# Performance work log

Measured on AMD Instinct MI355X. Metric: run time of the kernel, lower is better.

## Reference

```python
import jax, jax.numpy as jnp
import numpy as np

N = 20000      # nodes per batched graph
E = 320000     # directed edges per batched graph
F_IN = 128     # num_features
H = 256        # nhid == each gnn filter
G = 128        # number of graphs in batch


def setup_inputs() -> dict:
    key = jax.random.key(0)
    ks = jax.random.split(key, 24)

    def glorot(k, shape):
        fan_in, fan_out = shape[0], shape[1]
        limit = np.sqrt(6.0 / (fan_in + fan_out)).astype(np.float32)
        return jax.random.uniform(k, shape, jnp.float32, -limit, limit)

    inp = {
        'x1': jax.random.normal(ks[0], (N, F_IN), jnp.float32),
        'x2': jax.random.normal(ks[1], (N, F_IN), jnp.float32),
        'edge_index1': jax.random.randint(ks[2], (2, E), 0, N),
        'edge_index2': jax.random.randint(ks[3], (2, E), 0, N),
        'batch1': jnp.sort(jax.random.randint(ks[4], (N,), 0, G)),
        'batch2': jnp.sort(jax.random.randint(ks[5], (N,), 0, G)),
        # GCN layer weights (shared between the two graphs, as in the module)
        'W0': glorot(ks[6], (F_IN, H)), 'b0': jnp.zeros((H,), jnp.float32),
        'W1': glorot(ks[7], (H, H)),    'b1': jnp.zeros((H,), jnp.float32),
        'W2': glorot(ks[8], (H, H)),    'b2': jnp.zeros((H,), jnp.float32),
        # MLP head: nhid*2 -> nhid -> nhid//2 -> 1
        'lw0': glorot(ks[9], (2 * H, H)),      'lb0': jnp.zeros((H,), jnp.float32),
        'lw1': glorot(ks[10], (H, H // 2)),    'lb1': jnp.zeros((H // 2,), jnp.float32),
        'lw2': glorot(ks[11], (H // 2, 1)),    'lb2': jnp.zeros((1,), jnp.float32),
    }
    return inp


def _gcn_conv(x, src, dst, W, b, n):
    """PyG GCNConv: x' = D^-1/2 (A + I) D^-1/2 (x W) + b (self-loops added)."""
    x = x @ W                                      # [N, out]
    loop = jnp.arange(n)
    s = jnp.concatenate([src, loop])               # sources incl. self-loops
    d = jnp.concatenate([dst, loop])               # targets incl. self-loops
    deg = jax.ops.segment_sum(jnp.ones(s.shape, jnp.float32), d, num_segments=n)
    dinv = jnp.where(deg > 0, deg ** -0.5, 0.0)
    norm = dinv[s] * dinv[d]                       # [E+N]
    out = jax.ops.segment_sum(x[s] * norm[:, None], d, num_segments=n)
    return out + b


def _encode(x, edge_index, batch, params):
    src, dst = edge_index[0], edge_index[1]
    n = x.shape[0]
    for (W, b) in params:
        # conv -> relu -> dropout(eval: identity)
        x = jax.nn.relu(_gcn_conv(x, src, dst, W, b, n))
    # global_add_pool
    return jax.ops.segment_sum(x, batch, num_segments=G)   # [G, H]


def reference(x1, x2, W0, b0, W1, b1, W2, b2,
              lw0, lb0, lw1, lb1, lw2, lb2,
              edge_index1, edge_index2, batch1, batch2):
    params = ((W0, b0), (W1, b1), (W2, b2))
    g1 = _encode(x1, edge_index1, batch1, params)
    g2 = _encode(x2, edge_index2, batch2, params)
    scores = jnp.concatenate([g1, g2], axis=1)              # [G, 2H]
    h = jax.nn.relu(scores @ lw0 + lb0)
    h = jax.nn.relu(h @ lw1 + lb1)
    return jax.nn.sigmoid(h @ lw2 + lb2).reshape(-1)        # [G]
```

## Files before the change

kernel.cpp:

```cpp
#include <hip/hip_runtime.h>
#include <hip/hip_bf16.h>
#include <math.h>

#define HD 256
#define GB 128

typedef __attribute__((ext_vector_type(8))) short bf16x8;
typedef __attribute__((ext_vector_type(4))) float f32x4;
typedef __attribute__((ext_vector_type(2))) float f32x2;

__device__ __forceinline__ float bf2f(unsigned short u) {
  return __uint_as_float(((unsigned int)u) << 16);
}
__device__ __forceinline__ unsigned short f2bf(float f) {
  unsigned int u = __float_as_uint(f);
  unsigned int r = u + 0x7FFFu + ((u >> 16) & 1u);
  return (unsigned short)(r >> 16);
}

__device__ __forceinline__ float f8dec(unsigned u) {
  unsigned s = (u >> 7) & 1u, e = (u >> 3) & 15u, m = u & 7u;
  float mag = e ? __uint_as_float(((e + 120u) << 23) | (m << 20))
                : (float)m * 0.001953125f;
  return s ? -mag : mag;
}
__device__ __forceinline__ unsigned f8enc(float x) {
#if __has_builtin(__builtin_amdgcn_cvt_pk_fp8_f32)
  return (unsigned)__builtin_amdgcn_cvt_pk_fp8_f32(x, x, 0, false) & 0xFFu;
#else
  float a = fabsf(x);
  unsigned s = x < 0.f ? 0x80u : 0u;
  if (a >= 440.f) return s | 0x7Eu;
  if (a < 0.015625f) {
    int q = (int)rintf(a * 512.f);
    return s | (unsigned)q;
  }
  unsigned u = __float_as_uint(a);
  u += 0x7FFFFu + ((u >> 20) & 1u);
  unsigned e = (u >> 23) - 120u;
  if (e >= 16u) return s | 0x7Eu;
  return s | (e << 3) | ((u >> 20) & 7u);
#endif
}

template<int FB>
__device__ __forceinline__ void load_row_f8(const unsigned char* p, float (&f)[FB]) {
  if constexpr (FB == 4) {
    unsigned u = *(const unsigned*)p;
#if __has_builtin(__builtin_amdgcn_cvt_pk_f32_fp8)
    f32x2 lo = __builtin_amdgcn_cvt_pk_f32_fp8((int)u, false);
    f32x2 hi = __builtin_amdgcn_cvt_pk_f32_fp8((int)u, true);
    f[0] = lo[0]; f[1] = lo[1]; f[2] = hi[0]; f[3] = hi[1];
#else
    f[0] = f8dec(u); f[1] = f8dec(u >> 8); f[2] = f8dec(u >> 16); f[3] = f8dec(u >> 24);
#endif
  } else {
    unsigned u = *(const unsigned short*)p;
#if __has_builtin(__builtin_amdgcn_cvt_pk_f32_fp8)
    f32x2 lo = __builtin_amdgcn_cvt_pk_f32_fp8((int)u, false);
    f[0] = lo[0]; f[1] = lo[1];
#else
    f[0] = f8dec(u); f[1] = f8dec(u >> 8);
#endif
  }
}

__global__ __launch_bounds__(256) void k_prep(const float* __restrict__ W0, const float* __restrict__ W1,
                                              const float* __restrict__ W2,
                                              unsigned short* __restrict__ Wt0,
                                              unsigned short* __restrict__ Wt1,
                                              unsigned short* __restrict__ Wt2,
                                              const float4* __restrict__ x1, const float4* __restrict__ x2,
                                              unsigned* __restrict__ x8, int n4,
                                              float* __restrict__ scores, int* __restrict__ deg, int nd) {
  int i = blockIdx.x * blockDim.x + threadIdx.x;
  if (i < 163840) {
    const float* W; unsigned short* Wt; int j;
    if (i < 32768)      { W = W0; Wt = Wt0; j = i; }
    else if (i < 98304) { W = W1; Wt = Wt1; j = i - 32768; }
    else                { W = W2; Wt = Wt2; j = i - 98304; }
    int k = j >> 8, c = j & 255;
    Wt[(((size_t)(k >> 3) * HD) + c) * 8 + (k & 7)] = f2bf(W[(size_t)k * HD + c]);
    return;
  }
  int j = i - 163840;
  if (j < 2 * n4) {
    float4 v = (j < n4) ? x1[j] : x2[j - n4];
    x8[j] = f8enc(v.x) | (f8enc(v.y) << 8) | (f8enc(v.z) << 16) | (f8enc(v.w) << 24);
    return;
  }
  j -= 2 * n4;
  if (j < GB * 512) { scores[j] = 0.f; return; }
  j -= GB * 512;
  if (j < nd) deg[j] = 0;
}

__global__ void k_deg2(const int* __restrict__ dst1, const int* __restrict__ dst2,
                       int* __restrict__ deg, int e, int n0) {
  int i = blockIdx.x * blockDim.x + threadIdx.x;
  if (i >= 2 * e) return;
  int d = (i < e) ? dst1[i] : (dst2[i - e] + n0);
  atomicAdd(&deg[d], 1);
}

__global__ __launch_bounds__(256) void k_scan_a(const int* __restrict__ deg,
                                                int* __restrict__ partial, int n) {
  __shared__ int sh[256];
  int i = blockIdx.x * 256 + threadIdx.x;
  int v = (i < n) ? deg[i] : 0;
  sh[threadIdx.x] = v;
  __syncthreads();
#pragma unroll
  for (int off = 128; off; off >>= 1) {
    if (threadIdx.x < off) sh[threadIdx.x] += sh[threadIdx.x + off];
    __syncthreads();
  }
  if (threadIdx.x == 0) partial[blockIdx.x] = sh[0];
}

__global__ __launch_bounds__(256) void k_scan_b(int* __restrict__ partial, int nb,
                                                int* __restrict__ row_ptr, int n, int e_total) {
  __shared__ int sh[256];
  int t = threadIdx.x;
  int v = (t < nb) ? partial[t] : 0;
  sh[t] = v;
  __syncthreads();
#pragma unroll
  for (int off = 1; off < 256; off <<= 1) {
    int u = (t >= off) ? sh[t - off] : 0;
    __syncthreads();
    sh[t] += u;
    __syncthreads();
  }
  if (t < nb) partial[t] = sh[t] - v;
  if (t == 0) row_ptr[n] = e_total;
}

__global__ __launch_bounds__(256) void k_scan_c(const int* __restrict__ deg,
                                                const int* __restrict__ partial,
                                                int* __restrict__ row_ptr,
                                                float* __restrict__ dinv,
                                                int* __restrict__ cursor, int n) {
  __shared__ int sh[256];
  int i = blockIdx.x * 256 + threadIdx.x;
  int t = threadIdx.x;
  int v = (i < n) ? deg[i] : 0;
  sh[t] = v;
  __syncthreads();
#pragma unroll
  for (int off = 1; off < 256; off <<= 1) {
    int u = (t >= off) ? sh[t - off] : 0;
    __syncthreads();
    sh[t] += u;
    __syncthreads();
  }
  if (i < n) {
    row_ptr[i] = sh[t] - v + partial[blockIdx.x];
    dinv[i] = rsqrtf((float)(v + 1));
    cursor[i] = 0;
  }
}

__global__ void k_build2(const int* __restrict__ ei1, const int* __restrict__ ei2,
                         const float* __restrict__ dinv, const int* __restrict__ row_ptr,
                         int* __restrict__ cursor, int2* __restrict__ csr, int e, int n0) {
  int i = blockIdx.x * blockDim.x + threadIdx.x;
  if (i >= 2 * e) return;
  int s, d;
  if (i < e) { s = ei1[i];          d = ei1[i + e]; }
  else       { s = ei2[i - e] + n0; d = ei2[i] + n0; }
  int pos = atomicAdd(&cursor[d], 1);
  int idx = row_ptr[d] + pos;
  csr[idx] = make_int2(s, __float_as_int(dinv[s] * dinv[d]));
}

template<bool BR, bool F8OUT>
__global__ __launch_bounds__(256) void k_gemm_bf(const unsigned short* __restrict__ A,
                                                 const unsigned short* __restrict__ Wt,
                                                 const float* __restrict__ bias,
                                                 void* __restrict__ Cv,
                                                 int K) {
  const int w = threadIdx.x >> 6;
  const int lane = threadIdx.x & 63;
  const int bm = blockIdx.x * 64 + w * 16;
  const int bn = blockIdx.y * 128;
  const int row = bm + (lane & 15);
  const int kg0 = lane >> 4;
  f32x4 acc[8];
#pragma unroll
  for (int i = 0; i < 8; ++i) acc[i] = (f32x4){0.f, 0.f, 0.f, 0.f};

  const unsigned short* arow = A + (size_t)row * K + kg0 * 8;
  for (int k0 = 0; k0 < K; k0 += 32) {
    bf16x8 a = *(const bf16x8*)(arow + k0);
    const unsigned short* bbase =
        Wt + (((size_t)((k0 >> 3) + kg0) * HD) + bn + (lane & 15)) * 8;
#pragma unroll
    for (int nt = 0; nt < 8; ++nt) {
      bf16x8 b = *(const bf16x8*)(bbase + (size_t)nt * 16 * 8);
      acc[nt] = __builtin_amdgcn_mfma_f32_16x16x32_bf16(a, b, acc[nt], 0, 0, 0);
    }
  }
  const int crow = bm + (lane >> 4) * 4;
  const int ccol = bn + (lane & 15);
#pragma unroll
  for (int nt = 0; nt < 8; ++nt) {
    float bb = BR ? bias[ccol + nt * 16] : 0.f;
#pragma unroll
    for (int r = 0; r < 4; ++r) {
      float v = acc[nt][r];
      if (BR) v = fmaxf(v + bb, 0.f);
      size_t idx = (size_t)(crow + r) * HD + ccol + nt * 16;
      if constexpr (F8OUT) ((unsigned char*)Cv)[idx] = (unsigned char)f8enc(v);
      else                 ((unsigned short*)Cv)[idx] = f2bf(v);
    }
  }
}

template<int FB, bool BR>
__global__ __launch_bounds__(256) void k_gathf8(const unsigned char* __restrict__ y,
                                                const int* __restrict__ row_ptr,
                                                const int2* __restrict__ csr,
                                                const float* __restrict__ dinv,
                                                const float* __restrict__ bias,
                                                unsigned short* __restrict__ out, int n) {
  constexpr int F = FB * 64;
  int node = (blockIdx.x * blockDim.x + threadIdx.x) >> 6;
  int lane = threadIdx.x & 63;
  if (node >= n) return;
  float di = dinv[node];
  float c = di * di;
  float self[FB], acc0[FB], acc1[FB];
  load_row_f8<FB>(y + (size_t)node * F + lane * FB, self);
#pragma unroll
  for (int q = 0; q < FB; ++q) { acc0[q] = c * self[q]; acc1[q] = 0.f; }

  int e = row_ptr[node], end = row_ptr[node + 1];
  while (e < end) {
    int cnt = min(end - e, 64);
    int2 ew = make_int2(0, 0);
    if (lane < cnt) ew = csr[e + lane];
    int j = 0;
    for (; j + 4 <= cnt; j += 4) {
      int s0 = __shfl(ew.x, j + 0), s1 = __shfl(ew.x, j + 1);
      int s2 = __shfl(ew.x, j + 2), s3 = __shfl(ew.x, j + 3);
      float w0 = __int_as_float(__shfl(ew.y, j + 0));
      float w1 = __int_as_float(__shfl(ew.y, j + 1));
      float w2 = __int_as_float(__shfl(ew.y, j + 2));
      float w3 = __int_as_float(__shfl(ew.y, j + 3));
      float r0[FB], r1[FB], r2[FB], r3[FB];
      load_row_f8<FB>(y + (size_t)s0 * F + lane * FB, r0);
      load_row_f8<FB>(y + (size_t)s1 * F + lane * FB, r1);
      load_row_f8<FB>(y + (size_t)s2 * F + lane * FB, r2);
      load_row_f8<FB>(y + (size_t)s3 * F + lane * FB, r3);
#pragma unroll
      for (int q = 0; q < FB; ++q) {
        acc0[q] = fmaf(w0, r0[q], acc0[q]);
        acc1[q] = fmaf(w1, r1[q], acc1[q]);
        acc0[q] = fmaf(w2, r2[q], acc0[q]);
        acc1[q] = fmaf(w3, r3[q], acc1[q]);
      }
    }
    for (; j < cnt; ++j) {
      int s0 = __shfl(ew.x, j);
      float w0 = __int_as_float(__shfl(ew.y, j));
      float r0[FB];
      load_row_f8<FB>(y + (size_t)s0 * F + lane * FB, r0);
#pragma unroll
      for (int q = 0; q < FB; ++q) acc0[q] = fmaf(w0, r0[q], acc0[q]);
    }
    e += cnt;
  }
  unsigned short o[FB];
#pragma unroll
  for (int q = 0; q < FB; ++q) {
    float v = acc0[q] + acc1[q];
    if (BR) v = fmaxf(v + bias[lane * FB + q], 0.f);
    o[q] = f2bf(v);
  }
  if constexpr (FB == 4) {
    ushort4 ov; ov.x = o[0]; ov.y = o[1]; ov.z = o[2]; ov.w = o[3];
    *(ushort4*)(out + (size_t)node * F + lane * FB) = ov;
  } else {
    ushort2 ov; ov.x = o[0]; ov.y = o[1];
    *(ushort2*)(out + (size_t)node * F + lane * FB) = ov;
  }
}

__global__ __launch_bounds__(256) void k_pool4(const unsigned short* __restrict__ h,
                                               const int* __restrict__ batch1,
                                               const int* __restrict__ batch2,
                                               float* __restrict__ scores,
                                               int n, int n0) {
  int wave = (blockIdx.x * blockDim.x + threadIdx.x) >> 6;
  int lane = threadIdx.x & 63;
  int beg = wave * 32;
  if (beg >= n) return;
  int end = min(beg + 32, n);
  bool g1 = beg >= n0;
  const int* bat = g1 ? batch2 : batch1;
  int boff = g1 ? n0 : 0;
  int coff = g1 ? HD : 0;
  float ax = 0.f, ay = 0.f, az = 0.f, aw = 0.f;
  int cur = bat[beg - boff];
  for (int i = beg; i < end; ++i) {
    int b = bat[i - boff];
    if (b != cur) {
      float* srow = &scores[(size_t)cur * 512 + coff + lane * 4];
      atomicAdd(&srow[0], ax); atomicAdd(&srow[1], ay);
      atomicAdd(&srow[2], az); atomicAdd(&srow[3], aw);
      ax = ay = az = aw = 0.f;
      cur = b;
    }
    ushort4 v = reinterpret_cast<const ushort4*>(h + (size_t)i * HD)[lane];
    ax += bf2f(v.x); ay += bf2f(v.y); az += bf2f(v.z); aw += bf2f(v.w);
  }
  float* srow = &scores[(size_t)cur * 512 + coff + lane * 4];
  atomicAdd(&srow[0], ax); atomicAdd(&srow[1], ay);
  atomicAdd(&srow[2], az); atomicAdd(&srow[3], aw);
}

__global__ __launch_bounds__(256) void k_head_a(const float* __restrict__ scores,
                                                const float* __restrict__ lw0,
                                                const float* __restrict__ lb0,
                                                float* __restrict__ h1) {
  __shared__ float s_in[512];
  __shared__ float part[4][64];
  const int r = blockIdx.x, ct = blockIdx.y;
  const int t = threadIdx.x;
  s_in[t]       = scores[(size_t)r * 512 + t];
  s_in[t + 256] = scores[(size_t)r * 512 + t + 256];
  __syncthreads();
  const int l = t & 63, w = t >> 6;
  const int col = ct * 64 + l;
  float acc = 0.f;
  const float* wp = lw0 + (size_t)(w * 128) * 256 + col;
  const float* sp = s_in + w * 128;
#pragma unroll 8
  for (int k = 0; k < 128; ++k) acc = fmaf(sp[k], wp[(size_t)k * 256], acc);
  part[w][l] = acc;
  __syncthreads();
  if (t < 64) {
    float v = part[0][t] + part[1][t] + part[2][t] + part[3][t] + lb0[ct * 64 + t];
    h1[(size_t)r * 256 + ct * 64 + t] = fmaxf(v, 0.f);
  }
}

__global__ __launch_bounds__(256) void k_head_b(const float* __restrict__ h1,
                                                const float* __restrict__ lw1,
                                                const float* __restrict__ lb1,
                                                const float* __restrict__ lw2,
                                                const float* __restrict__ lb2,
                                                float* __restrict__ out) {
  __shared__ float s_in[256];
  __shared__ float part[2][128];
  __shared__ float s_h2[128];
  __shared__ float red[4];
  const int r = blockIdx.x;
  const int t = threadIdx.x;
  s_in[t] = h1[(size_t)r * 256 + t];
  __syncthreads();
  const int l = t & 127, w = t >> 7;
  float acc = 0.f;
  const float* wp = lw1 + (size_t)(w * 128) * 128 + l;
  const float* sp = s_in + w * 128;
#pragma unroll 8
  for (int k = 0; k < 128; ++k) acc = fmaf(sp[k], wp[(size_t)k * 128], acc);
  part[w][l] = acc;
  __syncthreads();
  if (t < 128) s_h2[t] = fmaxf(part[0][t] + part[1][t] + lb1[t], 0.f);
  __syncthreads();
  float p = (t < 128) ? s_h2[t] * lw2[t] : 0.f;
#pragma unroll
  for (int off = 32; off; off >>= 1) p += __shfl_down(p, off);
  if ((t & 63) == 0) red[t >> 6] = p;
  __syncthreads();
  if (t == 0) {
    float z = red[0] + red[1] + red[2] + red[3] + lb2[0];
    out[r] = 1.f / (1.f + expf(-z));
  }
}

extern "C" void kernel_launch(void* const* d_in, const int* in_sizes, int n_in,
                              void* d_out, int out_size, void* d_ws, size_t ws_size,
                              hipStream_t stream) {
  const float* x1 = (const float*)d_in[0];
  const float* x2 = (const float*)d_in[1];
  const int* ei1 = (const int*)d_in[2];
  const int* ei2 = (const int*)d_in[3];
  const int* batch1 = (const int*)d_in[4];
  const int* batch2 = (const int*)d_in[5];
  const float* W0 = (const float*)d_in[6];  const float* b0 = (const float*)d_in[7];
  const float* W1 = (const float*)d_in[8];  const float* b1 = (const float*)d_in[9];
  const float* W2 = (const float*)d_in[10]; const float* b2 = (const float*)d_in[11];
  const float* lw0 = (const float*)d_in[12]; const float* lb0 = (const float*)d_in[13];
  const float* lw1 = (const float*)d_in[14]; const float* lb1 = (const float*)d_in[15];
  const float* lw2 = (const float*)d_in[16]; const float* lb2 = (const float*)d_in[17];
  float* out = (float*)d_out;

  const int N = in_sizes[0] / 128;
  const int E = in_sizes[2] / 2;
  const int N2 = 2 * N, E2 = 2 * E;
  const int NB = (N2 + 255) / 256;

  char* p = (char*)d_ws;
  unsigned char*  x8   = (unsigned char*)p;  p += (size_t)N2 * 128;
  unsigned short* aggx = (unsigned short*)p; p += (size_t)N2 * 128 * 2;
  unsigned short* h    = (unsigned short*)p; p += (size_t)N2 * HD * 2;
  unsigned char*  y    = (unsigned char*)p;  p += (size_t)N2 * HD;
  unsigned short* Wt0  = (unsigned short*)p; p += (size_t)128 * HD * 2;
  unsigned short* Wt1  = (unsigned short*)p; p += (size_t)HD * HD * 2;
  unsigned short* Wt2  = (unsigned short*)p; p += (size_t)HD * HD * 2;
  float* dinv   = (float*)p; p += (size_t)N2 * 4;
  float* scores = (float*)p; p += (size_t)GB * 512 * 4;
  float* h1     = (float*)p; p += (size_t)GB * 256 * 4;
  int2* csr    = (int2*)p; p += (size_t)E2 * 8;
  int* deg     = (int*)p; p += (size_t)N2 * 4;
  int* row_ptr = (int*)p; p += (size_t)(N2 + 1) * 4;
  int* cursor  = (int*)p; p += (size_t)N2 * 4;
  int* partial = (int*)p; p += 256 * 4;

  int n4 = N * 128 / 4;
  int prep_total = 163840 + 2 * n4 + GB * 512 + N2;
  k_prep<<<(prep_total + 255) / 256, 256, 0, stream>>>(
      W0, W1, W2, Wt0, Wt1, Wt2,
      (const float4*)x1, (const float4*)x2, (unsigned*)x8, n4, scores, deg, N2);

  k_deg2<<<(2 * E + 255) / 256, 256, 0, stream>>>(ei1 + E, ei2 + E, deg, E, N);
  k_scan_a<<<NB, 256, 0, stream>>>(deg, partial, N2);
  k_scan_b<<<1, 256, 0, stream>>>(partial, NB, row_ptr, N2, E2);
  k_scan_c<<<NB, 256, 0, stream>>>(deg, partial, row_ptr, dinv, cursor, N2);
  k_build2<<<(2 * E + 255) / 256, 256, 0, stream>>>(ei1, ei2, dinv, row_ptr,
                                                    cursor, csr, E, N);

  dim3 ggrid(N2 / 64, 2);
  k_gathf8<2, false><<<(N2 + 3) / 4, 256, 0, stream>>>(x8, row_ptr, csr, dinv,
                                                       nullptr, aggx, N2);
  k_gemm_bf<true, false><<<ggrid, 256, 0, stream>>>(aggx, Wt0, b0, h, 128);
  k_gemm_bf<false, true><<<ggrid, 256, 0, stream>>>(h, Wt1, nullptr, y, HD);
  k_gathf8<4, true><<<(N2 + 3) / 4, 256, 0, stream>>>(y, row_ptr, csr, dinv,
                                                      b1, h, N2);
  k_gemm_bf<false, true><<<ggrid, 256, 0, stream>>>(h, Wt2, nullptr, y, HD);
  k_gathf8<4, true><<<(N2 + 3) / 4, 256, 0, stream>>>(y, row_ptr, csr, dinv,
                                                      b2, h, N2);

  int waves = N2 / 32;
  k_pool4<<<(waves + 3) / 4, 256, 0, stream>>>(h, batch1, batch2, scores, N2, N);

  dim3 hgrid(GB, 4);
  k_head_a<<<hgrid, 256, 0, stream>>>(scores, lw0, lb0, h1);
  k_head_b<<<GB, 256, 0, stream>>>(h1, lw1, lb1, lw2, lb2, out);
}
```

Baseline: 239.3 us.

## Use single-pass decoupled-lookback scan, 2x row GEMM tiles, and 8-way gather unroll

Replaces the three-kernel degree scan with one kernel that uses a ticket counter and decoupled lookback to chain block prefixes. The GEMM now computes 32 rows per wave, two MFMA row tiles sharing each B load, with bounds clamping. The gather loop is unrolled to 8 neighbors per step so more loads are in flight. Together these cut two launches, halve B-operand traffic per output, and raise memory-level parallelism, at the cost of more registers and spin-waiting in the scan.

```diff
diff --git a/kernel.cpp b/kernel.cpp
--- a/kernel.cpp
+++ b/kernel.cpp
@@ -72,7 +72,8 @@
                                               unsigned short* __restrict__ Wt2,
                                               const float4* __restrict__ x1, const float4* __restrict__ x2,
                                               unsigned* __restrict__ x8, int n4,
-                                              float* __restrict__ scores, int* __restrict__ deg, int nd) {
+                                              float* __restrict__ scores, int* __restrict__ deg, int nd,
+                                              int* __restrict__ sstate, int ns) {
   int i = blockIdx.x * blockDim.x + threadIdx.x;
   if (i < 163840) {
     const float* W; unsigned short* Wt; int j;
@@ -92,7 +93,9 @@
   j -= 2 * n4;
   if (j < GB * 512) { scores[j] = 0.f; return; }
   j -= GB * 512;
-  if (j < nd) deg[j] = 0;
+  if (j < nd) { deg[j] = 0; return; }
+  j -= nd;
+  if (j < ns) sstate[j] = 0;
 }
 
 __global__ void k_deg2(const int* __restrict__ dst1, const int* __restrict__ dst2,
@@ -103,61 +106,63 @@
   atomicAdd(&deg[d], 1);
 }
 
-__global__ __launch_bounds__(256) void k_scan_a(const int* __restrict__ deg,
-                                                int* __restrict__ partial, int n) {
+__global__ __launch_bounds__(256) void k_scan1(const int* __restrict__ deg,
+                                               int* __restrict__ row_ptr,
+                                               float* __restrict__ dinv,
+                                               int* __restrict__ cursor,
+                                               int* __restrict__ ticket,
+                                               int* __restrict__ bflag,
+                                               int* __restrict__ bval,
+                                               int* __restrict__ bpre,
+                                               int n) {
   __shared__ int sh[256];
-  int i = blockIdx.x * 256 + threadIdx.x;
+  __shared__ int s_bid, s_prev;
+  int t = threadIdx.x;
+  if (t == 0) s_bid = atomicAdd(ticket, 1);
+  __syncthreads();
+  int bid = s_bid;
+  int i = bid * 256 + t;
   int v = (i < n) ? deg[i] : 0;
-  sh[threadIdx.x] = v;
-  __syncthreads();
-#pragma unroll
-  for (int off = 128; off; off >>= 1) {
-    if (threadIdx.x < off) sh[threadIdx.x] += sh[threadIdx.x + off];
-    __syncthreads();
-  }
-  if (threadIdx.x == 0) partial[blockIdx.x] = sh[0];
-}
-
-__global__ __launch_bounds__(256) void k_scan_b(int* __restrict__ partial, int nb,
-                                                int* __restrict__ row_ptr, int n, int e_total) {
-  __shared__ int sh[256];
-  int t = threadIdx.x;
-  int v = (t < nb) ? partial[t] : 0;
   sh[t] = v;
   __syncthreads();
-#pragma unroll
   for (int off = 1; off < 256; off <<= 1) {
     int u = (t >= off) ? sh[t - off] : 0;
     __syncthreads();
     sh[t] += u;
     __syncthreads();
   }
-  if (t < nb) partial[t] = sh[t] - v;
-  if (t == 0) row_ptr[n] = e_total;
-}
-
-__global__ __launch_bounds__(256) void k_scan_c(const int* __restrict__ deg,
-                                                const int* __restrict__ partial,
-                                                int* __restrict__ row_ptr,
-                                                float* __restrict__ dinv,
-                                                int* __restrict__ cursor, int n) {
-  __shared__ int sh[256];
-  int i = blockIdx.x * 256 + threadIdx.x;
-  int t = threadIdx.x;
-  int v = (i < n) ? deg[i] : 0;
-  sh[t] = v;
-  __syncthreads();
-#pragma unroll
-  for (int off = 1; off < 256; off <<= 1) {
-    int u = (t >= off) ? sh[t - off] : 0;
-    __syncthreads();
-    sh[t] += u;
-    __syncthreads();
-  }
+  if (t == 0) {
+    int total = sh[255];
+    int excl = 0;
+    if (bid > 0) {
+      atomicExch(&bval[bid], total);
+      __threadfence();
+      atomicExch(&bflag[bid], 1);
+      int pb = bid - 1;
+      while (true) {
+        int st;
+        do { st = atomicAdd(&bflag[pb], 0); } while (st == 0);
+        if (st == 2) { excl += atomicAdd(&bpre[pb], 0); break; }
+        excl += atomicAdd(&bval[pb], 0);
+        --pb;
+      }
+      atomicExch(&bpre[bid], excl + total);
+      __threadfence();
+      atomicExch(&bflag[bid], 2);
+    } else {
+      atomicExch(&bpre[0], total);
+      __threadfence();
+      atomicExch(&bflag[0], 2);
+    }
+    s_prev = excl;
+  }
+  __syncthreads();
+  int prev = s_prev;
   if (i < n) {
-    row_ptr[i] = sh[t] - v + partial[blockIdx.x];
+    row_ptr[i] = prev + sh[t] - v;
     dinv[i] = rsqrtf((float)(v + 1));
     cursor[i] = 0;
+    if (i == n - 1) row_ptr[n] = prev + sh[t];
   }
 }
 
@@ -179,40 +184,53 @@
                                                  const unsigned short* __restrict__ Wt,
                                                  const float* __restrict__ bias,
                                                  void* __restrict__ Cv,
-                                                 int K) {
+                                                 int K, int M) {
   const int w = threadIdx.x >> 6;
   const int lane = threadIdx.x & 63;
-  const int bm = blockIdx.x * 64 + w * 16;
+  const int bm = blockIdx.x * 128 + w * 32;
   const int bn = blockIdx.y * 128;
-  const int row = bm + (lane & 15);
+  const int rr = lane & 15;
   const int kg0 = lane >> 4;
-  f32x4 acc[8];
-#pragma unroll
-  for (int i = 0; i < 8; ++i) acc[i] = (f32x4){0.f, 0.f, 0.f, 0.f};
-
-  const unsigned short* arow = A + (size_t)row * K + kg0 * 8;
+  const int r0c = min(bm + rr, M - 1);
+  const int r1c = min(bm + 16 + rr, M - 1);
+  f32x4 acc[2][8];
+#pragma unroll
+  for (int h = 0; h < 2; ++h)
+#pragma unroll
+    for (int i = 0; i < 8; ++i) acc[h][i] = (f32x4){0.f, 0.f, 0.f, 0.f};
+
+  const unsigned short* a0 = A + (size_t)r0c * K + kg0 * 8;
+  const unsigned short* a1 = A + (size_t)r1c * K + kg0 * 8;
   for (int k0 = 0; k0 < K; k0 += 32) {
-    bf16x8 a = *(const bf16x8*)(arow + k0);
+    bf16x8 av0 = *(const bf16x8*)(a0 + k0);
+    bf16x8 av1 = *(const bf16x8*)(a1 + k0);
     const unsigned short* bbase =
-        Wt + (((size_t)((k0 >> 3) + kg0) * HD) + bn + (lane & 15)) * 8;
+        Wt + (((size_t)((k0 >> 3) + kg0) * HD) + bn + rr) * 8;
 #pragma unroll
     for (int nt = 0; nt < 8; ++nt) {
       bf16x8 b = *(const bf16x8*)(bbase + (size_t)nt * 16 * 8);
-      acc[nt] = __builtin_amdgcn_mfma_f32_16x16x32_bf16(a, b, acc[nt], 0, 0, 0);
+      acc[0][nt] = __builtin_amdgcn_mfma_f32_16x16x32_bf16(av0, b, acc[0][nt], 0, 0, 0);
+      acc[1][nt] = __builtin_amdgcn_mfma_f32_16x16x32_bf16(av1, b, acc[1][nt], 0, 0, 0);
     }
   }
   const int crow = bm + (lane >> 4) * 4;
-  const int ccol = bn + (lane & 15);
-#pragma unroll
-  for (int nt = 0; nt < 8; ++nt) {
-    float bb = BR ? bias[ccol + nt * 16] : 0.f;
-#pragma unroll
-    for (int r = 0; r < 4; ++r) {
-      float v = acc[nt][r];
-      if (BR) v = fmaxf(v + bb, 0.f);
-      size_t idx = (size_t)(crow + r) * HD + ccol + nt * 16;
-      if constexpr (F8OUT) ((unsigned char*)Cv)[idx] = (unsigned char)f8enc(v);
-      else                 ((unsigned short*)Cv)[idx] = f2bf(v);
+  const int ccol = bn + rr;
+#pragma unroll
+  for (int h = 0; h < 2; ++h) {
+#pragma unroll
+    for (int nt = 0; nt < 8; ++nt) {
+      float bb = BR ? bias[ccol + nt * 16] : 0.f;
+#pragma unroll
+      for (int r = 0; r < 4; ++r) {
+        int row = crow + h * 16 + r;
+        if (row < M) {
+          float v = acc[h][nt][r];
+          if (BR) v = fmaxf(v + bb, 0.f);
+          size_t idx = (size_t)row * HD + ccol + nt * 16;
+          if constexpr (F8OUT) ((unsigned char*)Cv)[idx] = (unsigned char)f8enc(v);
+          else                 ((unsigned short*)Cv)[idx] = f2bf(v);
+        }
+      }
     }
   }
 }
@@ -241,24 +259,24 @@
     int2 ew = make_int2(0, 0);
     if (lane < cnt) ew = csr[e + lane];
     int j = 0;
-    for (; j + 4 <= cnt; j += 4) {
-      int s0 = __shfl(ew.x, j + 0), s1 = __shfl(ew.x, j + 1);
-      int s2 = __shfl(ew.x, j + 2), s3 = __shfl(ew.x, j + 3);
-      float w0 = __int_as_float(__shfl(ew.y, j + 0));
-      float w1 = __int_as_float(__shfl(ew.y, j + 1));
-      float w2 = __int_as_float(__shfl(ew.y, j + 2));
-      float w3 = __int_as_float(__shfl(ew.y, j + 3));
-      float r0[FB], r1[FB], r2[FB], r3[FB];
-      load_row_f8<FB>(y + (size_t)s0 * F + lane * FB, r0);
-      load_row_f8<FB>(y + (size_t)s1 * F + lane * FB, r1);
-      load_row_f8<FB>(y + (size_t)s2 * F + lane * FB, r2);
-      load_row_f8<FB>(y + (size_t)s3 * F + lane * FB, r3);
-#pragma unroll
-      for (int q = 0; q < FB; ++q) {
-        acc0[q] = fmaf(w0, r0[q], acc0[q]);
-        acc1[q] = fmaf(w1, r1[q], acc1[q]);
-        acc0[q] = fmaf(w2, r2[q], acc0[q]);
-        acc1[q] = fmaf(w3, r3[q], acc1[q]);
+    for (; j + 8 <= cnt; j += 8) {
+      int s[8]; float wt[8];
+#pragma unroll
+      for (int q = 0; q < 8; ++q) {
+        s[q] = __shfl(ew.x, j + q);
+        wt[q] = __int_as_float(__shfl(ew.y, j + q));
+      }
+      float r[8][FB];
+#pragma unroll
+      for (int q = 0; q < 8; ++q)
+        load_row_f8<FB>(y + (size_t)s[q] * F + lane * FB, r[q]);
+#pragma unroll
+      for (int q = 0; q < 8; q += 2) {
+#pragma unroll
+        for (int d = 0; d < FB; ++d) {
+          acc0[d] = fmaf(wt[q], r[q][d], acc0[d]);
+          acc1[d] = fmaf(wt[q + 1], r[q + 1][d], acc1[d]);
+        }
       }
     }
     for (; j < cnt; ++j) {
@@ -418,29 +436,32 @@
   int* deg     = (int*)p; p += (size_t)N2 * 4;
   int* row_ptr = (int*)p; p += (size_t)(N2 + 1) * 4;
   int* cursor  = (int*)p; p += (size_t)N2 * 4;
-  int* partial = (int*)p; p += 256 * 4;
+  int* ticket  = (int*)p; p += 4;
+  int* bflag   = (int*)p; p += (size_t)NB * 4;
+  int* bval    = (int*)p; p += (size_t)NB * 4;
+  int* bpre    = (int*)p; p += (size_t)NB * 4;
 
   int n4 = N * 128 / 4;
-  int prep_total = 163840 + 2 * n4 + GB * 512 + N2;
+  int ns = 1 + NB;
+  int prep_total = 163840 + 2 * n4 + GB * 512 + N2 + ns;
   k_prep<<<(prep_total + 255) / 256, 256, 0, stream>>>(
       W0, W1, W2, Wt0, Wt1, Wt2,
-      (const float4*)x1, (const float4*)x2, (unsigned*)x8, n4, scores, deg, N2);
+      (const float4*)x1, (const float4*)x2, (unsigned*)x8, n4, scores, deg, N2,
+      ticket, ns);
 
   k_deg2<<<(2 * E + 255) / 256, 256, 0, stream>>>(ei1 + E, ei2 + E, deg, E, N);
-  k_scan_a<<<NB, 256, 0, stream>>>(deg, partial, N2);
-  k_scan_b<<<1, 256, 0, stream>>>(partial, NB, row_ptr, N2, E2);
-  k_scan_c<<<NB, 256, 0, stream>>>(deg, partial, row_ptr, dinv, cursor, N2);
+  k_scan1<<<NB, 256, 0, stream>>>(deg, row_ptr, dinv, cursor, ticket, bflag, bval, bpre, N2);
   k_build2<<<(2 * E + 255) / 256, 256, 0, stream>>>(ei1, ei2, dinv, row_ptr,
                                                     cursor, csr, E, N);
 
-  dim3 ggrid(N2 / 64, 2);
+  dim3 ggrid((N2 + 127) / 128, 2);
   k_gathf8<2, false><<<(N2 + 3) / 4, 256, 0, stream>>>(x8, row_ptr, csr, dinv,
                                                        nullptr, aggx, N2);
-  k_gemm_bf<true, false><<<ggrid, 256, 0, stream>>>(aggx, Wt0, b0, h, 128);
-  k_gemm_bf<false, true><<<ggrid, 256, 0, stream>>>(h, Wt1, nullptr, y, HD);
+  k_gemm_bf<true, false><<<ggrid, 256, 0, stream>>>(aggx, Wt0, b0, h, 128, N2);
+  k_gemm_bf<false, true><<<ggrid, 256, 0, stream>>>(h, Wt1, nullptr, y, HD, N2);
   k_gathf8<4, true><<<(N2 + 3) / 4, 256, 0, stream>>>(y, row_ptr, csr, dinv,
                                                       b1, h, N2);
-  k_gemm_bf<false, true><<<ggrid, 256, 0, stream>>>(h, Wt2, nullptr, y, HD);
+  k_gemm_bf<false, true><<<ggrid, 256, 0, stream>>>(h, Wt2, nullptr, y, HD, N2);
   k_gathf8<4, true><<<(N2 + 3) / 4, 256, 0, stream>>>(y, row_ptr, csr, dinv,
                                                       b2, h, N2);
 
```

After: 260.0 us. 8.6% more time.
